# Optimization experiments

Measured on AMD Instinct MI355X. Metric: run time of the kernel, lower is better.

The kernel has to match this reference:

```python
import jax, jax.numpy as jnp
import numpy as np

B, T, C = 2, 2048, 2048
H = 16
D = C // H  # head_size = 128
ROPE_BASE = 10000.0


def _rope_cos_sin(seq_len, dim, dtype=jnp.float32):
    # torchtune RotaryPositionalEmbeddings: interleaved pair rotation
    inv_freq = 1.0 / (ROPE_BASE ** (jnp.arange(0, dim, 2, dtype=jnp.float32) / dim))  # [D/2]
    ang = jnp.arange(seq_len, dtype=jnp.float32)[:, None] * inv_freq[None, :]  # [T, D/2]
    return jnp.cos(ang).astype(dtype), jnp.sin(ang).astype(dtype)


def _apply_rope(x, cos, sin):
    # x: [B, T, H, D]; rotate interleaved pairs (even, odd)
    x1 = x[..., 0::2]
    x2 = x[..., 1::2]
    c = cos[None, :, None, :]
    s = sin[None, :, None, :]
    out = jnp.stack([x1 * c - x2 * s, x1 * s + x2 * c], axis=-1)  # [B,T,H,D/2,2]
    return out.reshape(x.shape)


def setup_inputs() -> dict:
    key = jax.random.key(0)
    ks = jax.random.split(key, 5)
    scale = 1.0 / np.sqrt(C)
    return {
        "x": jax.random.normal(ks[0], (B, T, C), jnp.float32),
        "W_attn": jax.random.normal(ks[1], (C, 3 * C), jnp.float32) * scale,
        "b_attn": jax.random.normal(ks[2], (3 * C,), jnp.float32) * 0.01,
        "W_proj": jax.random.normal(ks[3], (C, C), jnp.float32) * scale,
        "b_proj": jax.random.normal(ks[4], (C,), jnp.float32) * 0.01,
    }


def reference(x, W_attn, b_attn, W_proj, b_proj):
    b, t, c = x.shape
    qkv = x @ W_attn + b_attn                      # [B,T,3C]
    q, k, v = jnp.split(qkv, 3, axis=-1)
    q = q.reshape(b, t, H, D)
    k = k.reshape(b, t, H, D)
    v = v.reshape(b, t, H, D)
    cos, sin = _rope_cos_sin(t, D, x.dtype)
    q = _apply_rope(q, cos, sin)
    k = _apply_rope(k, cos, sin)
    # [B,H,T,D]
    q = q.transpose(0, 2, 1, 3)
    k = k.transpose(0, 2, 1, 3)
    v = v.transpose(0, 2, 1, 3)
    scores = jnp.einsum("bhqd,bhkd->bhqk", q, k) / jnp.sqrt(jnp.asarray(D, x.dtype))
    causal = jnp.tril(jnp.ones((t, t), dtype=bool))  # [T,T]
    scores = jnp.where(causal[None, None], scores, jnp.asarray(-jnp.inf, scores.dtype))
    probs = jax.nn.softmax(scores, axis=-1)
    out = jnp.einsum("bhqk,bhkd->bhqd", probs, v)  # [B,H,T,D]
    out = out.transpose(0, 2, 1, 3).reshape(b, t, c)
    return out @ W_proj + b_proj
```

## Files before the change

kernel.cpp:

```cpp
#include <hip/hip_runtime.h>
#include <hip/hip_bf16.h>
#include <math.h>

#define B_ 2
#define T_ 2048
#define C_ 2048
#define H_ 16
#define D_ 128
#define M_ (B_ * T_)
#define N3C (3 * C_)

typedef __attribute__((ext_vector_type(8))) short v8s;
typedef __attribute__((ext_vector_type(4))) float v4f;

typedef const __attribute__((address_space(1))) void* gas_t;
typedef __attribute__((address_space(3))) void* las_t;

__device__ __forceinline__ void gl16(const void* g, void* l) {
  __builtin_amdgcn_global_load_lds((gas_t)g, (las_t)l, 16, 0, 0);
}

__device__ inline unsigned short f2bf(float f) {
  unsigned u = __builtin_bit_cast(unsigned, f);
  u += 0x7FFFu + ((u >> 16) & 1u);
  return (unsigned short)(u >> 16);
}
__device__ inline float bf2f(unsigned short h) {
  unsigned u = (unsigned)h << 16;
  return __builtin_bit_cast(float, u);
}

__global__ __launch_bounds__(256) void split_rows(
    const float* __restrict__ X, unsigned short* __restrict__ XH,
    unsigned short* __restrict__ XL) {
  const long i4 = ((long)blockIdx.x * 256 + threadIdx.x) * 4;
  float4 v = *(const float4*)(X + i4);
  ushort4 hh, ll;
  hh.x = f2bf(v.x); ll.x = f2bf(v.x - bf2f(hh.x));
  hh.y = f2bf(v.y); ll.y = f2bf(v.y - bf2f(hh.y));
  hh.z = f2bf(v.z); ll.z = f2bf(v.z - bf2f(hh.z));
  hh.w = f2bf(v.w); ll.w = f2bf(v.w - bf2f(hh.w));
  *(ushort4*)&XH[i4] = hh;
  *(ushort4*)&XL[i4] = ll;
}

__global__ __launch_bounds__(256) void convert_wT(
    const float* __restrict__ W, unsigned short* __restrict__ WH,
    unsigned short* __restrict__ WL, int K, int N) {
  __shared__ float Ts[64][68];
  const int tid = threadIdx.x;
  const int n0 = blockIdx.x * 64;
  const int k0 = blockIdx.y * 64;
#pragma unroll
  for (int it = 0; it < 4; ++it) {
    int f = it * 256 + tid;
    int r = f >> 4;
    int c4 = (f & 15) * 4;
    float4 v = *(const float4*)(W + (long)(k0 + r) * N + n0 + c4);
    *(float4*)&Ts[r][c4] = v;
  }
  __syncthreads();
#pragma unroll
  for (int it = 0; it < 4; ++it) {
    int f = it * 256 + tid;
    int rn = f >> 4;
    int c4 = (f & 15) * 4;
    float x0 = Ts[c4 + 0][rn];
    float x1 = Ts[c4 + 1][rn];
    float x2 = Ts[c4 + 2][rn];
    float x3 = Ts[c4 + 3][rn];
    ushort4 hh, ll;
    hh.x = f2bf(x0); ll.x = f2bf(x0 - bf2f(hh.x));
    hh.y = f2bf(x1); ll.y = f2bf(x1 - bf2f(hh.y));
    hh.z = f2bf(x2); ll.z = f2bf(x2 - bf2f(hh.z));
    hh.w = f2bf(x3); ll.w = f2bf(x3 - bf2f(hh.w));
    long o = (long)(n0 + rn) * K + k0 + c4;
    *(ushort4*)&WH[o] = hh;
    *(ushort4*)&WL[o] = ll;
  }
}

__global__ __launch_bounds__(256) void gemm_pre_mfma(
    const unsigned short* __restrict__ AH, const unsigned short* __restrict__ AL,
    const unsigned short* __restrict__ BH, const unsigned short* __restrict__ BL,
    const float* __restrict__ bias, float* __restrict__ C, int K, int N) {
  __shared__ unsigned short smem[2 * 4 * 4096];

  const int tid = threadIdx.x;
  const int lane = tid & 63;
  const int w = tid >> 6;
  const int lm = lane & 15;
  const int quad = lane >> 4;

  const int gx = gridDim.x;
  const int lin = blockIdx.y * gx + blockIdx.x;
  const int pid_m = (lin & 7) + ((lin >> 3) / gx) * 8;
  const int pid_n = (lin >> 3) % gx;
  const int bm = pid_m * 128;
  const int bn = pid_n * 128;

  const int wm = (w & 1) * 64;
  const int wn = (w >> 1) * 64;

  const int srow = 32 * w + (lane >> 2);
  const int scol = ((lane & 3) ^ ((lane >> 3) & 3)) * 8;
  const unsigned short* pAH0 = AH + (size_t)(bm + srow) * K + scol;
  const unsigned short* pAH1 = pAH0 + (size_t)16 * K;
  const unsigned short* pAL0 = AL + (size_t)(bm + srow) * K + scol;
  const unsigned short* pAL1 = pAL0 + (size_t)16 * K;
  const unsigned short* pBH0 = BH + (size_t)(bn + srow) * K + scol;
  const unsigned short* pBH1 = pBH0 + (size_t)16 * K;
  const unsigned short* pBL0 = BL + (size_t)(bn + srow) * K + scol;
  const unsigned short* pBL1 = pBL0 + (size_t)16 * K;

#define STAGE(base, kk) do {                                      \
    unsigned short* d_ = (base) + 1024 * w;                       \
    const int ko_ = (kk) * 32;                                    \
    gl16(pAH0 + ko_, d_);                                         \
    gl16(pAH1 + ko_, d_ + 512);                                   \
    gl16(pAL0 + ko_, d_ + 4096);                                  \
    gl16(pAL1 + ko_, d_ + 4096 + 512);                            \
    gl16(pBH0 + ko_, d_ + 8192);                                  \
    gl16(pBH1 + ko_, d_ + 8192 + 512);                            \
    gl16(pBL0 + ko_, d_ + 12288);                                 \
    gl16(pBL1 + ko_, d_ + 12288 + 512);                           \
  } while (0)

  v4f acc[4][4];
#pragma unroll
  for (int i = 0; i < 4; ++i)
#pragma unroll
    for (int j = 0; j < 4; ++j) {
      v4f z = {0.f, 0.f, 0.f, 0.f};
      acc[i][j] = z;
    }

  const int kswz = (quad ^ ((lm >> 1) & 3)) * 8;

  const int nk = K >> 5;
  unsigned short* sb = smem;
  unsigned short* nb = smem + 16384;

  STAGE(sb, 0);

  for (int t = 0; t < nk; ++t) {
    __syncthreads();

    if (t + 1 < nk) STAGE(nb, t + 1);

    const unsigned short* sAH = sb;
    const unsigned short* sAL = sb + 4096;
    const unsigned short* sBH = sb + 8192;
    const unsigned short* sBL = sb + 12288;

    v8s aH[4], aL[4], bHf[4], bLf[4];
#pragma unroll
    for (int mt = 0; mt < 4; ++mt) {
      const int r = wm + mt * 16 + lm;
      aH[mt] = *(const v8s*)&sAH[r * 32 + kswz];
      aL[mt] = *(const v8s*)&sAL[r * 32 + kswz];
    }
#pragma unroll
    for (int nt = 0; nt < 4; ++nt) {
      const int r = wn + nt * 16 + lm;
      bHf[nt] = *(const v8s*)&sBH[r * 32 + kswz];
      bLf[nt] = *(const v8s*)&sBL[r * 32 + kswz];
    }

    __builtin_amdgcn_s_setprio(1);
#pragma unroll
    for (int mt = 0; mt < 4; ++mt)
#pragma unroll
      for (int nt = 0; nt < 4; ++nt) {
        acc[mt][nt] = __builtin_amdgcn_mfma_f32_16x16x32_bf16(aH[mt], bHf[nt], acc[mt][nt], 0, 0, 0);
        acc[mt][nt] = __builtin_amdgcn_mfma_f32_16x16x32_bf16(aH[mt], bLf[nt], acc[mt][nt], 0, 0, 0);
        acc[mt][nt] = __builtin_amdgcn_mfma_f32_16x16x32_bf16(aL[mt], bHf[nt], acc[mt][nt], 0, 0, 0);
      }
    __builtin_amdgcn_s_setprio(0);

    unsigned short* tmp = sb; sb = nb; nb = tmp;
  }
#undef STAGE

  __syncthreads();
  float* eps = (float*)smem;
  float* myeps = eps + w * 1088;

  float bv[4];
#pragma unroll
  for (int nt = 0; nt < 4; ++nt) bv[nt] = bias[bn + wn + nt * 16 + lm];

  const int r2 = lane >> 2;
  const int c4 = (lane & 3) * 4;
#pragma unroll
  for (int mt = 0; mt < 4; ++mt) {
#pragma unroll
    for (int nt = 0; nt < 4; ++nt)
#pragma unroll
      for (int r = 0; r < 4; ++r)
        myeps[(quad * 4 + r) * 68 + nt * 16 + lm] = acc[mt][nt][r] + bv[nt];
    float* dst = C + (size_t)(bm + wm + mt * 16 + r2) * N + bn + wn + c4;
#pragma unroll
    for (int i = 0; i < 4; ++i) {
      float4 v = *(float4*)&myeps[r2 * 68 + c4 + i * 16];
      *(float4*)&dst[i * 16] = v;
    }
  }
}

__global__ __launch_bounds__(256) void rope_split(
    const float* __restrict__ qkv,
    unsigned short* __restrict__ QH, unsigned short* __restrict__ QL,
    unsigned short* __restrict__ KH, unsigned short* __restrict__ KL,
    unsigned short* __restrict__ VTH, unsigned short* __restrict__ VTL) {
  const int tb = blockIdx.x;
  const int h = blockIdx.y;
  const int b = blockIdx.z;
  const int tid = threadIdx.x;

  __shared__ unsigned short VH_s[128][66];
  __shared__ unsigned short VL_s[128][66];

  for (int part = 0; part < 2; ++part) {
    unsigned short* OH = part ? KH : QH;
    unsigned short* OL = part ? KL : QL;
    const float sc = part ? 1.0f : 0.12751879523595298f;
    const size_t colbase = (size_t)part * C_ + (size_t)h * D_;
#pragma unroll 2
    for (int it = 0; it < 16; ++it) {
      int f = it * 256 + tid;
      int r = f >> 6;
      int i = f & 63;
      int t = tb * 64 + r;
      float inv = exp2f(-(float)i * (13.28771237954945f / 64.0f));
      float ang = (float)t * inv;
      float s, c;
      sincosf(ang, &s, &c);
      const float* src = qkv + (size_t)(b * T_ + t) * N3C + colbase + 2 * i;
      float2 x = *(const float2*)src;
      float ox = (x.x * c - x.y * s) * sc;
      float oy = (x.x * s + x.y * c) * sc;
      size_t dst = ((size_t)(b * H_ + h) * T_ + t) * D_ + 2 * i;
      unsigned short hx = f2bf(ox), hy = f2bf(oy);
      ushort2 hh; hh.x = hx; hh.y = hy;
      *(ushort2*)&OH[dst] = hh;
      ushort2 ll; ll.x = f2bf(ox - bf2f(hx)); ll.y = f2bf(oy - bf2f(hy));
      *(ushort2*)&OL[dst] = ll;
    }
  }

#pragma unroll
  for (int it = 0; it < 8; ++it) {
    int f = it * 256 + tid;
    int r = f >> 5;
    int d4 = (f & 31) * 4;
    float4 v = *(const float4*)(qkv + (size_t)(b * T_ + tb * 64 + r) * N3C + 2 * C_ + h * D_ + d4);
    float vv[4] = {v.x, v.y, v.z, v.w};
#pragma unroll
    for (int j = 0; j < 4; ++j) {
      unsigned short hi = f2bf(vv[j]);
      VH_s[d4 + j][r] = hi;
      VL_s[d4 + j][r] = f2bf(vv[j] - bf2f(hi));
    }
  }
  __syncthreads();
#pragma unroll
  for (int it = 0; it < 4; ++it) {
    int f = it * 256 + tid;
    int d = f >> 3;
    int c8 = (f & 7) * 8;
    size_t dst = ((size_t)(b * H_ + h) * D_ + d) * T_ + tb * 64 + c8;
    unsigned short th[8], tl[8];
#pragma unroll
    for (int j = 0; j < 8; ++j) { th[j] = VH_s[d][c8 + j]; tl[j] = VL_s[d][c8 + j]; }
    *(uint4*)&VTH[dst] = *(uint4*)th;
    *(uint4*)&VTL[dst] = *(uint4*)tl;
  }
}

__global__ __launch_bounds__(512, 4) void attn_mfma(
    const unsigned short* __restrict__ QH, const unsigned short* __restrict__ QL,
    const unsigned short* __restrict__ KH, const unsigned short* __restrict__ KL,
    const unsigned short* __restrict__ VTH, const unsigned short* __restrict__ VTL,
    unsigned short* __restrict__ OHp, unsigned short* __restrict__ OLp) {
  const int qb = (int)gridDim.x - 1 - (int)blockIdx.x;
  const int h = blockIdx.y;
  const int b = blockIdx.z;
  const int tid = threadIdx.x;
  const int lane = tid & 63;
  const int w = tid >> 6;
  const int lm = lane & 15;
  const int quad = lane >> 4;

  __shared__ unsigned short KS_H[32][136], KS_L[32][136];
  __shared__ unsigned short VS_H[128][40], VS_L[128][40];
  __shared__ unsigned short PS_H[128][40], PS_L[128][40];

  const size_t qbase = ((size_t)(b * H_ + h) * T_ + qb * 128 + w * 16 + lm) * D_;
  v8s qh[4], ql[4];
#pragma unroll
  for (int ks = 0; ks < 4; ++ks) {
    qh[ks] = *(const v8s*)&QH[qbase + ks * 32 + quad * 8];
    ql[ks] = *(const v8s*)&QL[qbase + ks * 32 + quad * 8];
  }

  v8s ones;
#pragma unroll
  for (int j = 0; j < 8; ++j) ones[j] = (short)0x3F80;

  const int kr = tid >> 4;
  const int kc = (tid & 15) * 8;
  const int vd = tid >> 2;
  const int vc = (tid & 3) * 8;

  const size_t kbase0 = (size_t)(b * H_ + h) * T_ * D_;
  const size_t vbase0 = (size_t)(b * H_ + h) * D_ * T_;
  const int nkb = 4 * qb + 4;

  uint4 khp = *(const uint4*)&KH[kbase0 + (size_t)kr * D_ + kc];
  uint4 klp = *(const uint4*)&KL[kbase0 + (size_t)kr * D_ + kc];
  uint4 vhp = *(const uint4*)&VTH[vbase0 + (size_t)vd * T_ + vc];
  uint4 vlp = *(const uint4*)&VTL[vbase0 + (size_t)vd * T_ + vc];

  v4f acc_o[8], acc_l;
#pragma unroll
  for (int nt = 0; nt < 8; ++nt) {
    v4f z = {0.f, 0.f, 0.f, 0.f};
    acc_o[nt] = z;
  }
  {
    v4f z = {0.f, 0.f, 0.f, 0.f};
    acc_l = z;
  }

  const float M2 = 32.0f;

  for (int kb = 0; kb < nkb; ++kb) {
    __syncthreads();
    *(uint4*)&KS_H[kr][kc] = khp;
    *(uint4*)&KS_L[kr][kc] = klp;
    *(uint4*)&VS_H[vd][vc] = vhp;
    *(uint4*)&VS_L[vd][vc] = vlp;
    __syncthreads();

    if (kb + 1 < nkb) {
      size_t kg = kbase0 + (size_t)((kb + 1) * 32 + kr) * D_ + kc;
      khp = *(const uint4*)&KH[kg];
      klp = *(const uint4*)&KL[kg];
      size_t vg = vbase0 + (size_t)vd * T_ + (kb + 1) * 32 + vc;
      vhp = *(const uint4*)&VTH[vg];
      vlp = *(const uint4*)&VTL[vg];
    }

    v4f s0, s1;
    {
      v4f z = {0.f, 0.f, 0.f, 0.f};
      s0 = z; s1 = z;
    }
#pragma unroll
    for (int ks = 0; ks < 4; ++ks) {
      int k8 = ks * 32 + quad * 8;
      v8s bh0 = *(const v8s*)&KS_H[lm][k8];
      v8s bl0 = *(const v8s*)&KS_L[lm][k8];
      v8s bh1 = *(const v8s*)&KS_H[16 + lm][k8];
      v8s bl1 = *(const v8s*)&KS_L[16 + lm][k8];
      s0 = __builtin_amdgcn_mfma_f32_16x16x32_bf16(qh[ks], bh0, s0, 0, 0, 0);
      s1 = __builtin_amdgcn_mfma_f32_16x16x32_bf16(qh[ks], bh1, s1, 0, 0, 0);
      s0 = __builtin_amdgcn_mfma_f32_16x16x32_bf16(qh[ks], bl0, s0, 0, 0, 0);
      s1 = __builtin_amdgcn_mfma_f32_16x16x32_bf16(qh[ks], bl1, s1, 0, 0, 0);
      s0 = __builtin_amdgcn_mfma_f32_16x16x32_bf16(ql[ks], bh0, s0, 0, 0, 0);
      s1 = __builtin_amdgcn_mfma_f32_16x16x32_bf16(ql[ks], bh1, s1, 0, 0, 0);
    }

#pragma unroll
    for (int r = 0; r < 4; ++r) {
      int rowg = qb * 128 + w * 16 + quad * 4 + r;
      float v0 = (kb * 32 + lm > rowg) ? -INFINITY : s0[r];
      float v1 = (kb * 32 + 16 + lm > rowg) ? -INFINITY : s1[r];
      float p0 = __builtin_amdgcn_exp2f(v0 - M2);
      float p1 = __builtin_amdgcn_exp2f(v1 - M2);

      int prow = w * 16 + quad * 4 + r;
      unsigned short p0h = f2bf(p0);
      PS_H[prow][lm] = p0h;
      PS_L[prow][lm] = f2bf(p0 - bf2f(p0h));
      unsigned short p1h = f2bf(p1);
      PS_H[prow][16 + lm] = p1h;
      PS_L[prow][16 + lm] = f2bf(p1 - bf2f(p1h));
    }

    v8s ph = *(const v8s*)&PS_H[w * 16 + lm][quad * 8];
    v8s pl = *(const v8s*)&PS_L[w * 16 + lm][quad * 8];
    acc_l = __builtin_amdgcn_mfma_f32_16x16x32_bf16(ph, ones, acc_l, 0, 0, 0);
    acc_l = __builtin_amdgcn_mfma_f32_16x16x32_bf16(pl, ones, acc_l, 0, 0, 0);
#pragma unroll
    for (int nt = 0; nt < 8; ++nt) {
      v8s vh = *(const v8s*)&VS_H[nt * 16 + lm][quad * 8];
      v8s vl = *(const v8s*)&VS_L[nt * 16 + lm][quad * 8];
      acc_o[nt] = __builtin_amdgcn_mfma_f32_16x16x32_bf16(ph, vh, acc_o[nt], 0, 0, 0);
      acc_o[nt] = __builtin_amdgcn_mfma_f32_16x16x32_bf16(ph, vl, acc_o[nt], 0, 0, 0);
      acc_o[nt] = __builtin_amdgcn_mfma_f32_16x16x32_bf16(pl, vh, acc_o[nt], 0, 0, 0);
    }
  }

#pragma unroll
  for (int r = 0; r < 4; ++r) {
    float invl = 1.0f / acc_l[r];
    size_t row = (size_t)(b * T_ + qb * 128 + w * 16 + quad * 4 + r);
#pragma unroll
    for (int nt = 0; nt < 8; ++nt) {
      float o = acc_o[nt][r] * invl;
      unsigned short oh = f2bf(o);
      size_t idx = row * C_ + h * D_ + nt * 16 + lm;
      OHp[idx] = oh;
      OLp[idx] = f2bf(o - bf2f(oh));
    }
  }
}

extern "C" void kernel_launch(void* const* d_in, const int* in_sizes, int n_in,
                              void* d_out, int out_size, void* d_ws, size_t ws_size,
                              hipStream_t stream) {
  const float* x      = (const float*)d_in[0];
  const float* W_attn = (const float*)d_in[1];
  const float* b_attn = (const float*)d_in[2];
  const float* W_proj = (const float*)d_in[3];
  const float* b_proj = (const float*)d_in[4];
  float* out = (float*)d_out;

  char* wsb = (char*)d_ws;
  const size_t MiB = 1048576;
  float* qkv = (float*)wsb;
  unsigned short* WtaH = (unsigned short*)(wsb + 96 * MiB);
  unsigned short* WtaL = (unsigned short*)(wsb + 120 * MiB);
  unsigned short* XH   = (unsigned short*)(wsb + 144 * MiB);
  unsigned short* XL   = (unsigned short*)(wsb + 160 * MiB);
  unsigned short* QH   = (unsigned short*)(wsb + 96 * MiB);
  unsigned short* QL   = (unsigned short*)(wsb + 112 * MiB);
  unsigned short* KH   = (unsigned short*)(wsb + 128 * MiB);
  unsigned short* KL   = (unsigned short*)(wsb + 144 * MiB);
  unsigned short* VTH  = (unsigned short*)(wsb + 160 * MiB);
  unsigned short* VTL  = (unsigned short*)(wsb + 176 * MiB);
  unsigned short* WtpH = (unsigned short*)(wsb + 32 * MiB);
  unsigned short* WtpL = (unsigned short*)(wsb + 40 * MiB);
  unsigned short* AOH  = (unsigned short*)(wsb + 48 * MiB);
  unsigned short* AOL  = (unsigned short*)(wsb + 64 * MiB);

  convert_wT<<<dim3(N3C / 64, C_ / 64), 256, 0, stream>>>(W_attn, WtaH, WtaL, C_, N3C);
  split_rows<<<dim3((M_ * C_) / 1024), 256, 0, stream>>>(x, XH, XL);
  gemm_pre_mfma<<<dim3(N3C / 128, M_ / 128), 256, 0, stream>>>(
      XH, XL, WtaH, WtaL, b_attn, qkv, C_, N3C);
  rope_split<<<dim3(T_ / 64, H_, B_), 256, 0, stream>>>(qkv, QH, QL, KH, KL, VTH, VTL);
  convert_wT<<<dim3(C_ / 64, C_ / 64), 256, 0, stream>>>(W_proj, WtpH, WtpL, C_, C_);
  attn_mfma<<<dim3(T_ / 128, H_, B_), 512, 0, stream>>>(
      QH, QL, KH, KL, VTH, VTL, AOH, AOL);
  gemm_pre_mfma<<<dim3(C_ / 128, M_ / 128), 256, 0, stream>>>(
      AOH, AOL, WtpH, WtpL, b_proj, out, C_, C_);
}
```

Measured before the change: 740.3 us.

## Use 256x256 tile, 512-thread GEMM kernel for QKV projection

Adds a new split-bf16 MFMA GEMM kernel with 256x256 output tiles, 8 waves each computing 128x64, and grouped block ordering, then uses it for the QKV projection. Larger tiles raise arithmetic intensity and reuse of the A and B tiles loaded into LDS, cutting global and LDS traffic per FLOP. The cost is 128 KB of LDS for double buffering and many more accumulator registers, which may lower occupancy. The 3-pass bf16 error-compensation scheme is kept.

```diff
diff --git a/kernel.cpp b/kernel.cpp
--- a/kernel.cpp
+++ b/kernel.cpp
@@ -194,6 +194,132 @@
   const int c4 = (lane & 3) * 4;
 #pragma unroll
   for (int mt = 0; mt < 4; ++mt) {
+#pragma unroll
+    for (int nt = 0; nt < 4; ++nt)
+#pragma unroll
+      for (int r = 0; r < 4; ++r)
+        myeps[(quad * 4 + r) * 68 + nt * 16 + lm] = acc[mt][nt][r] + bv[nt];
+    float* dst = C + (size_t)(bm + wm + mt * 16 + r2) * N + bn + wn + c4;
+#pragma unroll
+    for (int i = 0; i < 4; ++i) {
+      float4 v = *(float4*)&myeps[r2 * 68 + c4 + i * 16];
+      *(float4*)&dst[i * 16] = v;
+    }
+  }
+}
+
+__global__ __launch_bounds__(512, 2) void gemm_pre_mfma_256(
+    const unsigned short* __restrict__ AH, const unsigned short* __restrict__ AL,
+    const unsigned short* __restrict__ BH, const unsigned short* __restrict__ BL,
+    const float* __restrict__ bias, float* __restrict__ C, int K, int N) {
+  __shared__ unsigned short smem[2 * 4 * 8192];
+
+  const int tid = threadIdx.x;
+  const int lane = tid & 63;
+  const int w = tid >> 6;
+  const int lm = lane & 15;
+  const int quad = lane >> 4;
+
+  const int gx = gridDim.x;
+  const int lin = blockIdx.y * gx + blockIdx.x;
+  const int pid_m = (lin & 7) + ((lin >> 3) / gx) * 8;
+  const int pid_n = (lin >> 3) % gx;
+  const int bm = pid_m * 256;
+  const int bn = pid_n * 256;
+
+  const int wm = (w & 1) * 128;
+  const int wn = (w >> 1) * 64;
+
+  const int srow = tid >> 2;
+  const int scol = ((tid & 3) ^ ((tid >> 3) & 3)) * 8;
+  const unsigned short* pAH0 = AH + (size_t)(bm + srow) * K + scol;
+  const unsigned short* pAH1 = pAH0 + (size_t)128 * K;
+  const unsigned short* pAL0 = AL + (size_t)(bm + srow) * K + scol;
+  const unsigned short* pAL1 = pAL0 + (size_t)128 * K;
+  const unsigned short* pBH0 = BH + (size_t)(bn + srow) * K + scol;
+  const unsigned short* pBH1 = pBH0 + (size_t)128 * K;
+  const unsigned short* pBL0 = BL + (size_t)(bn + srow) * K + scol;
+  const unsigned short* pBL1 = pBL0 + (size_t)128 * K;
+
+#define STAGE256(base, kk) do {                                   \
+    unsigned short* d_ = (base) + 512 * w;                        \
+    const int ko_ = (kk) * 32;                                    \
+    gl16(pAH0 + ko_, d_);                                         \
+    gl16(pAH1 + ko_, d_ + 4096);                                  \
+    gl16(pAL0 + ko_, d_ + 8192);                                  \
+    gl16(pAL1 + ko_, d_ + 8192 + 4096);                           \
+    gl16(pBH0 + ko_, d_ + 16384);                                 \
+    gl16(pBH1 + ko_, d_ + 16384 + 4096);                          \
+    gl16(pBL0 + ko_, d_ + 24576);                                 \
+    gl16(pBL1 + ko_, d_ + 24576 + 4096);                          \
+  } while (0)
+
+  v4f acc[8][4];
+#pragma unroll
+  for (int i = 0; i < 8; ++i)
+#pragma unroll
+    for (int j = 0; j < 4; ++j) {
+      v4f z = {0.f, 0.f, 0.f, 0.f};
+      acc[i][j] = z;
+    }
+
+  const int kswz = (quad ^ ((lm >> 1) & 3)) * 8;
+
+  const int nk = K >> 5;
+  unsigned short* sb = smem;
+  unsigned short* nb = smem + 32768;
+
+  STAGE256(sb, 0);
+
+  for (int t = 0; t < nk; ++t) {
+    __syncthreads();
+
+    if (t + 1 < nk) STAGE256(nb, t + 1);
+
+    const unsigned short* sAH = sb;
+    const unsigned short* sAL = sb + 8192;
+    const unsigned short* sBH = sb + 16384;
+    const unsigned short* sBL = sb + 24576;
+
+    v8s bHf[4], bLf[4];
+#pragma unroll
+    for (int nt = 0; nt < 4; ++nt) {
+      const int r = wn + nt * 16 + lm;
+      bHf[nt] = *(const v8s*)&sBH[r * 32 + kswz];
+      bLf[nt] = *(const v8s*)&sBL[r * 32 + kswz];
+    }
+
+    __builtin_amdgcn_s_setprio(1);
+#pragma unroll
+    for (int mt = 0; mt < 8; ++mt) {
+      const int r = wm + mt * 16 + lm;
+      v8s aH = *(const v8s*)&sAH[r * 32 + kswz];
+      v8s aL = *(const v8s*)&sAL[r * 32 + kswz];
+#pragma unroll
+      for (int nt = 0; nt < 4; ++nt) {
+        acc[mt][nt] = __builtin_amdgcn_mfma_f32_16x16x32_bf16(aH, bHf[nt], acc[mt][nt], 0, 0, 0);
+        acc[mt][nt] = __builtin_amdgcn_mfma_f32_16x16x32_bf16(aH, bLf[nt], acc[mt][nt], 0, 0, 0);
+        acc[mt][nt] = __builtin_amdgcn_mfma_f32_16x16x32_bf16(aL, bHf[nt], acc[mt][nt], 0, 0, 0);
+      }
+    }
+    __builtin_amdgcn_s_setprio(0);
+
+    unsigned short* tmp = sb; sb = nb; nb = tmp;
+  }
+#undef STAGE256
+
+  __syncthreads();
+  float* eps = (float*)smem;
+  float* myeps = eps + w * 1088;
+
+  float bv[4];
+#pragma unroll
+  for (int nt = 0; nt < 4; ++nt) bv[nt] = bias[bn + wn + nt * 16 + lm];
+
+  const int r2 = lane >> 2;
+  const int c4 = (lane & 3) * 4;
+#pragma unroll
+  for (int mt = 0; mt < 8; ++mt) {
 #pragma unroll
     for (int nt = 0; nt < 4; ++nt)
 #pragma unroll
@@ -448,7 +574,7 @@
 
   convert_wT<<<dim3(N3C / 64, C_ / 64), 256, 0, stream>>>(W_attn, WtaH, WtaL, C_, N3C);
   split_rows<<<dim3((M_ * C_) / 1024), 256, 0, stream>>>(x, XH, XL);
-  gemm_pre_mfma<<<dim3(N3C / 128, M_ / 128), 256, 0, stream>>>(
+  gemm_pre_mfma_256<<<dim3(N3C / 256, M_ / 256), 512, 0, stream>>>(
       XH, XL, WtaH, WtaL, b_attn, qkv, C_, N3C);
   rope_split<<<dim3(T_ / 64, H_, B_), 256, 0, stream>>>(qkv, QH, QL, KH, KL, VTH, VTL);
   convert_wT<<<dim3(C_ / 64, C_ / 64), 256, 0, stream>>>(W_proj, WtpH, WtpL, C_, C_);
```

After: 755.2 us. 2.0% more time.

## Replace QKV GEMM with 256x192-tile 8-wave kernel using phased prefetch

Applied to the files above, without the earlier changes.

Adds a new QKV projection GEMM kernel with 256x192 block tiles, 8 waves per block, double-buffered LDS and a swizzled layout. The global-to-LDS prefetch for the next K slice is split across four MFMA phases with barriers, and MFMA sections are raised to high priority. Blocks are remapped in groups of eight along M for L2 reuse. The goal is more data reuse and better overlap of loads with the split-bf16 (3-MFMA) compute, at the cost of higher register pressure and more barriers.

```diff
diff --git a/kernel.cpp b/kernel.cpp
--- a/kernel.cpp
+++ b/kernel.cpp
@@ -19,6 +19,7 @@
 __device__ __forceinline__ void gl16(const void* g, void* l) {
   __builtin_amdgcn_global_load_lds((gas_t)g, (las_t)l, 16, 0, 0);
 }
+__device__ __forceinline__ v8s ldv(const unsigned short* p) { return *(const v8s*)p; }
 
 __device__ inline unsigned short f2bf(float f) {
   unsigned u = __builtin_bit_cast(unsigned, f);
@@ -202,6 +203,155 @@
     float* dst = C + (size_t)(bm + wm + mt * 16 + r2) * N + bn + wn + c4;
 #pragma unroll
     for (int i = 0; i < 4; ++i) {
+      float4 v = *(float4*)&myeps[r2 * 68 + c4 + i * 16];
+      *(float4*)&dst[i * 16] = v;
+    }
+  }
+}
+
+#define BAR() do { asm volatile("" ::: "memory"); __builtin_amdgcn_s_barrier(); asm volatile("" ::: "memory"); } while (0)
+
+__global__ __launch_bounds__(512, 2) void gemm_qkv_8ph(
+    const unsigned short* __restrict__ AH, const unsigned short* __restrict__ AL,
+    const unsigned short* __restrict__ BH, const unsigned short* __restrict__ BL,
+    const float* __restrict__ bias, float* __restrict__ C, int K, int N) {
+  __shared__ unsigned short smem[2 * 28672];
+
+  const int tid = threadIdx.x;
+  const int lane = tid & 63;
+  const int w = tid >> 6;
+  const int lm = lane & 15;
+  const int quad = lane >> 4;
+
+  const int gx = gridDim.x;
+  const int lin = blockIdx.y * gx + blockIdx.x;
+  const int pid_m = (lin & 7) + ((lin >> 3) / gx) * 8;
+  const int pid_n = (lin >> 3) % gx;
+  const int bm = pid_m * 256;
+  const int bn = pid_n * 192;
+
+  const int wm = (w & 1) * 128;
+  const int wn = (w >> 1) * 48;
+
+  const unsigned short* aS[4]; int aD[4];
+#pragma unroll
+  for (int j = 0; j < 4; ++j) {
+    int g = tid + 512 * j;
+    int pl = g >> 10;
+    int p = g & 1023;
+    int row = p >> 2;
+    int c = (p & 3) ^ ((row >> 1) & 3);
+    aS[j] = (pl ? AL : AH) + (size_t)(bm + row) * K + c * 8;
+    aD[j] = pl * 8192 + p * 8;
+  }
+  const unsigned short* bS[3]; int bD[3];
+#pragma unroll
+  for (int j = 0; j < 3; ++j) {
+    int g = tid + 512 * j;
+    int pl = (g >= 768) ? 1 : 0;
+    int p = g - pl * 768;
+    int row = p >> 2;
+    int c = (p & 3) ^ ((row >> 1) & 3);
+    bS[j] = (pl ? BL : BH) + (size_t)(bn + row) * K + c * 8;
+    bD[j] = 16384 + pl * 6144 + p * 8;
+  }
+
+  v4f acc[8][3];
+#pragma unroll
+  for (int i = 0; i < 8; ++i)
+#pragma unroll
+    for (int j = 0; j < 3; ++j) {
+      v4f z = {0.f, 0.f, 0.f, 0.f};
+      acc[i][j] = z;
+    }
+
+  const int kswz = (quad ^ ((lm >> 1) & 3)) * 8;
+  const int nk = K >> 5;
+
+#pragma unroll
+  for (int j = 0; j < 4; ++j) gl16(aS[j], smem + aD[j]);
+#pragma unroll
+  for (int j = 0; j < 3; ++j) gl16(bS[j], smem + bD[j]);
+
+#define MM3(MT, NT, AH_, AL_)                                                           \
+  acc[MT][NT] = __builtin_amdgcn_mfma_f32_16x16x32_bf16(AH_, bh##NT, acc[MT][NT], 0, 0, 0); \
+  acc[MT][NT] = __builtin_amdgcn_mfma_f32_16x16x32_bf16(AH_, bl##NT, acc[MT][NT], 0, 0, 0); \
+  acc[MT][NT] = __builtin_amdgcn_mfma_f32_16x16x32_bf16(AL_, bh##NT, acc[MT][NT], 0, 0, 0);
+
+#define DO_PHASE(MA, MB, STAGES)                                              \
+  {                                                                           \
+    v8s xh = ldv(sbuf + (wm + (MA) * 16 + lm) * 32 + kswz);                   \
+    v8s xl = ldv(sbuf + 8192 + (wm + (MA) * 16 + lm) * 32 + kswz);            \
+    v8s yh = ldv(sbuf + (wm + (MB) * 16 + lm) * 32 + kswz);                   \
+    v8s yl = ldv(sbuf + 8192 + (wm + (MB) * 16 + lm) * 32 + kswz);            \
+    STAGES                                                                    \
+    BAR();                                                                    \
+    __builtin_amdgcn_s_setprio(1);                                            \
+    MM3(MA, 0, xh, xl) MM3(MA, 1, xh, xl) MM3(MA, 2, xh, xl)                  \
+    MM3(MB, 0, yh, yl) MM3(MB, 1, yh, yl) MM3(MB, 2, yh, yl)                  \
+    __builtin_amdgcn_s_setprio(0);                                            \
+    BAR();                                                                    \
+  }
+
+  for (int t = 0; t < nk; ++t) {
+    const unsigned short* sbuf = smem + (t & 1) * 28672;
+    unsigned short* nbuf = (unsigned short*)smem + ((t + 1) & 1) * 28672;
+    const int kn = (t + 1) * 32;
+    const bool pf = (t + 1 < nk);
+
+    if (pf) {
+      gl16(aS[0] + kn, nbuf + aD[0]);
+      gl16(aS[1] + kn, nbuf + aD[1]);
+      asm volatile("s_waitcnt vmcnt(2)" ::: "memory");
+    } else {
+      asm volatile("s_waitcnt vmcnt(0)" ::: "memory");
+    }
+    BAR();
+
+    v8s bh0 = ldv(sbuf + 16384 + (wn + lm) * 32 + kswz);
+    v8s bl0 = ldv(sbuf + 22528 + (wn + lm) * 32 + kswz);
+    v8s bh1 = ldv(sbuf + 16384 + (wn + 16 + lm) * 32 + kswz);
+    v8s bl1 = ldv(sbuf + 22528 + (wn + 16 + lm) * 32 + kswz);
+    v8s bh2 = ldv(sbuf + 16384 + (wn + 32 + lm) * 32 + kswz);
+    v8s bl2 = ldv(sbuf + 22528 + (wn + 32 + lm) * 32 + kswz);
+    {
+      v8s xh = ldv(sbuf + (wm + 0 * 16 + lm) * 32 + kswz);
+      v8s xl = ldv(sbuf + 8192 + (wm + 0 * 16 + lm) * 32 + kswz);
+      v8s yh = ldv(sbuf + (wm + 1 * 16 + lm) * 32 + kswz);
+      v8s yl = ldv(sbuf + 8192 + (wm + 1 * 16 + lm) * 32 + kswz);
+      __builtin_amdgcn_s_setprio(1);
+      MM3(0, 0, xh, xl) MM3(0, 1, xh, xl) MM3(0, 2, xh, xl)
+      MM3(1, 0, yh, yl) MM3(1, 1, yh, yl) MM3(1, 2, yh, yl)
+      __builtin_amdgcn_s_setprio(0);
+      BAR();
+    }
+    DO_PHASE(2, 3, if (pf) { gl16(aS[2] + kn, nbuf + aD[2]); gl16(aS[3] + kn, nbuf + aD[3]); })
+    DO_PHASE(4, 5, if (pf) { gl16(bS[0] + kn, nbuf + bD[0]); gl16(bS[1] + kn, nbuf + bD[1]); })
+    DO_PHASE(6, 7, if (pf) { gl16(bS[2] + kn, nbuf + bD[2]); })
+  }
+#undef DO_PHASE
+#undef MM3
+
+  __syncthreads();
+  float* eps = (float*)smem;
+  float* myeps = eps + w * 1088;
+
+  float bv[3];
+#pragma unroll
+  for (int nt = 0; nt < 3; ++nt) bv[nt] = bias[bn + wn + nt * 16 + lm];
+
+  const int r2 = lane >> 2;
+  const int c4 = (lane & 3) * 4;
+#pragma unroll
+  for (int mt = 0; mt < 8; ++mt) {
+#pragma unroll
+    for (int nt = 0; nt < 3; ++nt)
+#pragma unroll
+      for (int r = 0; r < 4; ++r)
+        myeps[(quad * 4 + r) * 68 + nt * 16 + lm] = acc[mt][nt][r] + bv[nt];
+    float* dst = C + (size_t)(bm + wm + mt * 16 + r2) * N + bn + wn + c4;
+#pragma unroll
+    for (int i = 0; i < 3; ++i) {
       float4 v = *(float4*)&myeps[r2 * 68 + c4 + i * 16];
       *(float4*)&dst[i * 16] = v;
     }
@@ -448,7 +598,7 @@
 
   convert_wT<<<dim3(N3C / 64, C_ / 64), 256, 0, stream>>>(W_attn, WtaH, WtaL, C_, N3C);
   split_rows<<<dim3((M_ * C_) / 1024), 256, 0, stream>>>(x, XH, XL);
-  gemm_pre_mfma<<<dim3(N3C / 128, M_ / 128), 256, 0, stream>>>(
+  gemm_qkv_8ph<<<dim3(N3C / 192, M_ / 256), 512, 0, stream>>>(
       XH, XL, WtaH, WtaL, b_attn, qkv, C_, N3C);
   rope_split<<<dim3(T_ / 64, H_, B_), 256, 0, stream>>>(qkv, QH, QL, KH, KL, VTH, VTL);
   convert_wT<<<dim3(C_ / 64, C_ / 64), 256, 0, stream>>>(W_proj, WtpH, WtpL, C_, C_);
```

After: 706.6 us. -4.6%, faster.
